# Performance work log

Measured on AMD Instinct MI355X. Metric: run time of the kernel, lower is better.

The kernel has to match this reference:

```python
import jax, jax.numpy as jnp
import numpy as np

B = 524288  # number of mel frames
MEL = 128   # mel bins (hard-coded in module)
D = 64      # code dim
K = 128     # codebook size


def setup_inputs() -> dict:
    key = jax.random.key(0)
    ks = jax.random.split(key, 7)
    return {
        "mel_frame": jax.random.normal(ks[0], (B, MEL), dtype=jnp.float32),
        "W_in": jax.random.normal(ks[1], (D, MEL), dtype=jnp.float32) * 0.05,
        "b_in": jax.random.normal(ks[2], (D,), dtype=jnp.float32) * 0.05,
        "cb0": jax.random.normal(ks[3], (K, D), dtype=jnp.float32),
        "cb1": jax.random.normal(ks[4], (K, D), dtype=jnp.float32),
        "W_out": jax.random.normal(ks[5], (MEL, D), dtype=jnp.float32) * 0.05,
        "b_out": jax.random.normal(ks[6], (MEL,), dtype=jnp.float32) * 0.05,
    }


def reference(mel_frame, W_in, b_in, cb0, cb1, W_out, b_out):
    # encode: project mel -> d, then greedy residual VQ over 2 codebooks
    z = mel_frame @ W_in.T + b_in                      # (B, D)
    residual = z
    z_q = jnp.zeros_like(z)
    idxs = []
    for cb in (cb0, cb1):
        # squared L2 distance without materializing (B, K, D):
        # ||r - c||^2 = ||r||^2 - 2 r.c + ||c||^2  -> (B, K)
        dist = (
            jnp.sum(residual * residual, axis=-1, keepdims=True)
            - 2.0 * (residual @ cb.T)
            + jnp.sum(cb * cb, axis=-1)
        )
        ind = jnp.argmin(dist, axis=-1)                # (B,)
        code = cb[ind]                                 # gather chosen codes (B, D)
        residual = residual - code
        z_q = z_q + code
        idxs.append(ind)
    # decode: sum of selected codes -> project back to mel
    mel = z_q @ W_out.T + b_out                        # (B, MEL)
    return mel, jnp.stack(idxs, axis=-1)
```

## Files before the change

### kernel.cpp

```cpp
#include <hip/hip_runtime.h>
#include <hip/hip_bf16.h>

#define B_ROWS   524288
#define MEL_BINS 128
#define DIM      64
#define KCODES   128

#define WS_WT 0
#define WS_P0 (WS_WT + MEL_BINS*DIM)
#define WS_P1 (WS_P0 + DIM*KCODES)
#define WS_N0 (WS_P1 + DIM*KCODES)
#define WS_N1 (WS_N0 + KCODES)
#define WS_T0 (WS_N1 + KCODES)
#define WS_T1 (WS_T0 + KCODES*MEL_BINS)
#define WS_TOT (WS_T1 + KCODES*MEL_BINS)

__device__ __forceinline__ float np_pairwise64_sq(const float* v) {
#pragma clang fp contract(off)
    float r0 = v[0]*v[0], r1 = v[1]*v[1], r2 = v[2]*v[2], r3 = v[3]*v[3];
    float r4 = v[4]*v[4], r5 = v[5]*v[5], r6 = v[6]*v[6], r7 = v[7]*v[7];
#pragma unroll
    for (int i = 8; i < 64; i += 8) {
        r0 += v[i+0]*v[i+0]; r1 += v[i+1]*v[i+1];
        r2 += v[i+2]*v[i+2]; r3 += v[i+3]*v[i+3];
        r4 += v[i+4]*v[i+4]; r5 += v[i+5]*v[i+5];
        r6 += v[i+6]*v[i+6]; r7 += v[i+7]*v[i+7];
    }
    return ((r0 + r1) + (r2 + r3)) + ((r4 + r5) + (r6 + r7));
}

__global__ __launch_bounds__(256) void rvq_precomp(
    const float* __restrict__ W_in, const float* __restrict__ cb0,
    const float* __restrict__ cb1, const float* __restrict__ W_out,
    float* __restrict__ ws)
{
#pragma clang fp contract(off)
    float* WT = ws + WS_WT;
    float* P0 = ws + WS_P0;
    float* P1 = ws + WS_P1;
    float* n0 = ws + WS_N0;
    float* n1 = ws + WS_N1;
    float* T0 = ws + WS_T0;
    float* T1 = ws + WS_T1;

    int tid = blockIdx.x * 256 + threadIdx.x;
    if (tid < 16384) {
        int i = tid >> 7, m = tid & 127;
        double a = 0.0;
        for (int d = 0; d < DIM; ++d)
            a = fma((double)cb0[i*DIM + d], (double)W_out[m*DIM + d], a);
        T0[tid] = (float)a;
    } else if (tid < 32768) {
        int t = tid - 16384;
        int i = t >> 7, m = t & 127;
        double a = 0.0;
        for (int d = 0; d < DIM; ++d)
            a = fma((double)cb1[i*DIM + d], (double)W_out[m*DIM + d], a);
        T1[t] = (float)a;
    } else if (tid < 40960) {
        int t = tid - 32768;
        int j = t >> 6, d = t & 63;
        WT[t] = W_in[d*MEL_BINS + j];
    } else if (tid < 41216) {
        int t = tid - 40960;
        const float* cb = (t & 128) ? cb1 : cb0;
        float*       nn = (t & 128) ? n1  : n0;
        int k = t & 127;
        nn[k] = np_pairwise64_sq(cb + k*DIM);
    } else if (tid < 49408) {
        int e = tid - 41216;
        int c = e >> 10, rem = e & 1023;
        int d = rem >> 4, t = rem & 15;
        P0[e] = cb0[(c*16 + t)*DIM + d];
    } else if (tid < 57600) {
        int e = tid - 49408;
        int c = e >> 10, rem = e & 1023;
        int d = rem >> 4, t = rem & 15;
        P1[e] = cb1[(c*16 + t)*DIM + d];
    }
}

__global__ __launch_bounds__(256) void rvq_main(
    const float* __restrict__ mel,
    const float* __restrict__ b_in,
    const float* __restrict__ cb0,
    const float* __restrict__ cb1,
    const float* __restrict__ b_out,
    const float* __restrict__ ws,
    float* __restrict__ out_mel,
    float* __restrict__ out_idx)
{
#pragma clang fp contract(off)
    const float* __restrict__ n0g = ws + WS_N0;
    const float* __restrict__ n1g = ws + WS_N1;
    const float* __restrict__ T0  = ws + WS_T0;
    const float* __restrict__ T1  = ws + WS_T1;

    __shared__ float slds[4096];
    float4* sw4 = reinterpret_cast<float4*>(slds);
    const float4* sl4 = reinterpret_cast<const float4*>(slds);

    const int tid = threadIdx.x;
    const int b = blockIdx.x * 256 + tid;
    const float4* melr = reinterpret_cast<const float4*>(mel + (size_t)b * MEL_BINS);

    float z[DIM];
#pragma unroll
    for (int d = 0; d < DIM; ++d) z[d] = 0.f;

    const float4* wt4 = reinterpret_cast<const float4*>(ws + WS_WT);
    for (int h = 0; h < 2; ++h) {
        __syncthreads();
#pragma unroll
        for (int i = 0; i < 4; ++i) sw4[i*256 + tid] = wt4[h*1024 + i*256 + tid];
        __syncthreads();

        for (int jc = 0; jc < 16; ++jc) {
            float4 m4 = melr[h*16 + jc];
#pragma unroll
            for (int seg = 0; seg < 4; ++seg) {
                float mj = (seg == 0) ? m4.x : (seg == 1) ? m4.y : (seg == 2) ? m4.z : m4.w;
                const float4* w4 = sl4 + (jc*4 + seg)*16;
#pragma unroll
                for (int q = 0; q < 16; ++q) {
                    float4 wv = w4[q];
                    z[4*q + 0] = fmaf(wv.x, mj, z[4*q + 0]);
                    z[4*q + 1] = fmaf(wv.y, mj, z[4*q + 1]);
                    z[4*q + 2] = fmaf(wv.z, mj, z[4*q + 2]);
                    z[4*q + 3] = fmaf(wv.w, mj, z[4*q + 3]);
                }
            }
        }
    }
#pragma unroll
    for (int d = 0; d < DIM; ++d) z[d] = z[d] + b_in[d];

    float s0 = z[0]*z[0], s1 = z[1]*z[1], s2 = z[2]*z[2], s3 = z[3]*z[3];
    float s4 = z[4]*z[4], s5 = z[5]*z[5], s6 = z[6]*z[6], s7 = z[7]*z[7];
#pragma unroll
    for (int i = 8; i < 64; i += 8) {
        s0 += z[i+0]*z[i+0]; s1 += z[i+1]*z[i+1];
        s2 += z[i+2]*z[i+2]; s3 += z[i+3]*z[i+3];
        s4 += z[i+4]*z[i+4]; s5 += z[i+5]*z[i+5];
        s6 += z[i+6]*z[i+6]; s7 += z[i+7]*z[i+7];
    }
    float sum_rr = ((s0 + s1) + (s2 + s3)) + ((s4 + s5) + (s6 + s7));

    const float4* p04 = reinterpret_cast<const float4*>(ws + WS_P0);
    float best0 = 3.4e38f; int i0 = 0;
    for (int h = 0; h < 2; ++h) {
        __syncthreads();
#pragma unroll
        for (int i = 0; i < 4; ++i) sw4[i*256 + tid] = p04[h*1024 + i*256 + tid];
        __syncthreads();

        for (int q = 0; q < 4; ++q) {
            const float4* pan = sl4 + q*256;
            float acc[16];
#pragma unroll
            for (int t = 0; t < 16; ++t) acc[t] = 0.f;
#pragma unroll
            for (int d = 0; d < DIM; ++d) {
                float4 p0 = pan[d*4 + 0];
                float4 p1 = pan[d*4 + 1];
                float4 p2 = pan[d*4 + 2];
                float4 p3 = pan[d*4 + 3];
                float zd = z[d];
                acc[ 0] = fmaf(p0.x, zd, acc[ 0]);
                acc[ 1] = fmaf(p0.y, zd, acc[ 1]);
                acc[ 2] = fmaf(p0.z, zd, acc[ 2]);
                acc[ 3] = fmaf(p0.w, zd, acc[ 3]);
                acc[ 4] = fmaf(p1.x, zd, acc[ 4]);
                acc[ 5] = fmaf(p1.y, zd, acc[ 5]);
                acc[ 6] = fmaf(p1.z, zd, acc[ 6]);
                acc[ 7] = fmaf(p1.w, zd, acc[ 7]);
                acc[ 8] = fmaf(p2.x, zd, acc[ 8]);
                acc[ 9] = fmaf(p2.y, zd, acc[ 9]);
                acc[10] = fmaf(p2.z, zd, acc[10]);
                acc[11] = fmaf(p2.w, zd, acc[11]);
                acc[12] = fmaf(p3.x, zd, acc[12]);
                acc[13] = fmaf(p3.y, zd, acc[13]);
                acc[14] = fmaf(p3.z, zd, acc[14]);
                acc[15] = fmaf(p3.w, zd, acc[15]);
            }
            const int kb = h*64 + q*16;
            const float* nk = n0g + kb;
#pragma unroll
            for (int t = 0; t < 16; ++t) {
                float dist = (sum_rr - 2.0f*acc[t]) + nk[t];
                if (dist < best0) { best0 = dist; i0 = kb + t; }
            }
        }
    }

    {
        const float* cc = cb0 + (size_t)i0 * DIM;
#pragma unroll
        for (int d = 0; d < DIM; ++d) z[d] = z[d] - cc[d];
    }

    s0 = z[0]*z[0]; s1 = z[1]*z[1]; s2 = z[2]*z[2]; s3 = z[3]*z[3];
    s4 = z[4]*z[4]; s5 = z[5]*z[5]; s6 = z[6]*z[6]; s7 = z[7]*z[7];
#pragma unroll
    for (int i = 8; i < 64; i += 8) {
        s0 += z[i+0]*z[i+0]; s1 += z[i+1]*z[i+1];
        s2 += z[i+2]*z[i+2]; s3 += z[i+3]*z[i+3];
        s4 += z[i+4]*z[i+4]; s5 += z[i+5]*z[i+5];
        s6 += z[i+6]*z[i+6]; s7 += z[i+7]*z[i+7];
    }
    sum_rr = ((s0 + s1) + (s2 + s3)) + ((s4 + s5) + (s6 + s7));

    const float4* p14 = reinterpret_cast<const float4*>(ws + WS_P1);
    float best1 = 3.4e38f; int i1 = 0;
    for (int h = 0; h < 2; ++h) {
        __syncthreads();
#pragma unroll
        for (int i = 0; i < 4; ++i) sw4[i*256 + tid] = p14[h*1024 + i*256 + tid];
        __syncthreads();

        for (int q = 0; q < 4; ++q) {
            const float4* pan = sl4 + q*256;
            float acc[16];
#pragma unroll
            for (int t = 0; t < 16; ++t) acc[t] = 0.f;
#pragma unroll
            for (int d = 0; d < DIM; ++d) {
                float4 p0 = pan[d*4 + 0];
                float4 p1 = pan[d*4 + 1];
                float4 p2 = pan[d*4 + 2];
                float4 p3 = pan[d*4 + 3];
                float zd = z[d];
                acc[ 0] = fmaf(p0.x, zd, acc[ 0]);
                acc[ 1] = fmaf(p0.y, zd, acc[ 1]);
                acc[ 2] = fmaf(p0.z, zd, acc[ 2]);
                acc[ 3] = fmaf(p0.w, zd, acc[ 3]);
                acc[ 4] = fmaf(p1.x, zd, acc[ 4]);
                acc[ 5] = fmaf(p1.y, zd, acc[ 5]);
                acc[ 6] = fmaf(p1.z, zd, acc[ 6]);
                acc[ 7] = fmaf(p1.w, zd, acc[ 7]);
                acc[ 8] = fmaf(p2.x, zd, acc[ 8]);
                acc[ 9] = fmaf(p2.y, zd, acc[ 9]);
                acc[10] = fmaf(p2.z, zd, acc[10]);
                acc[11] = fmaf(p2.w, zd, acc[11]);
                acc[12] = fmaf(p3.x, zd, acc[12]);
                acc[13] = fmaf(p3.y, zd, acc[13]);
                acc[14] = fmaf(p3.z, zd, acc[14]);
                acc[15] = fmaf(p3.w, zd, acc[15]);
            }
            const int kb = h*64 + q*16;
            const float* nk = n1g + kb;
#pragma unroll
            for (int t = 0; t < 16; ++t) {
                float dist = (sum_rr - 2.0f*acc[t]) + nk[t];
                if (dist < best1) { best1 = dist; i1 = kb + t; }
            }
        }
    }

    const float4* t0r = reinterpret_cast<const float4*>(T0 + (size_t)i0 * MEL_BINS);
    const float4* t1r = reinterpret_cast<const float4*>(T1 + (size_t)i1 * MEL_BINS);
    float4* outr = reinterpret_cast<float4*>(out_mel + (size_t)b * MEL_BINS);
#pragma unroll 4
    for (int q = 0; q < MEL_BINS / 4; ++q) {
        float4 a = t0r[q], cc = t1r[q];
        float4 o;
        o.x = a.x + cc.x + b_out[4*q + 0];
        o.y = a.y + cc.y + b_out[4*q + 1];
        o.z = a.z + cc.z + b_out[4*q + 2];
        o.w = a.w + cc.w + b_out[4*q + 3];
        outr[q] = o;
    }

    out_idx[2*(size_t)b + 0] = (float)i0;
    out_idx[2*(size_t)b + 1] = (float)i1;
}

extern "C" void kernel_launch(void* const* d_in, const int* in_sizes, int n_in,
                              void* d_out, int out_size, void* d_ws, size_t ws_size,
                              hipStream_t stream)
{
    const float* mel   = (const float*)d_in[0];
    const float* W_in  = (const float*)d_in[1];
    const float* b_in  = (const float*)d_in[2];
    const float* cb0   = (const float*)d_in[3];
    const float* cb1   = (const float*)d_in[4];
    const float* W_out = (const float*)d_in[5];
    const float* b_out = (const float*)d_in[6];

    float* ws      = (float*)d_ws;
    float* out_mel = (float*)d_out;
    float* out_idx = (float*)d_out + (size_t)B_ROWS * MEL_BINS;

    rvq_precomp<<<(WS_TOT + 255) / 256, 256, 0, stream>>>(W_in, cb0, cb1, W_out, ws);
    rvq_main<<<B_ROWS / 256, 256, 0, stream>>>(mel, b_in, cb0, cb1, b_out, ws,
                                               out_mel, out_idx);
}
```

Baseline: 516.5 us.

## Compute encoder projection in 16-dim chunks reading weights directly from global memory

The input projection no longer stages W_in^T through shared memory with block barriers. It loops over four 16-wide output-dim chunks, and each chunk re-reads the thread's mel row and takes uniform weight loads straight from the global workspace. This is meant to cut the live accumulator registers and remove the LDS staging and syncs, at the cost of reading the mel row four times, which relies on cache hits. The squared-norm reduction is folded into each chunk and rewritten with an 8-way accumulator array.

```diff
diff --git a/kernel.cpp b/kernel.cpp
--- a/kernel.cpp
+++ b/kernel.cpp
@@ -91,6 +91,7 @@
     float* __restrict__ out_idx)
 {
 #pragma clang fp contract(off)
+    const float* __restrict__ WTg = ws + WS_WT;
     const float* __restrict__ n0g = ws + WS_N0;
     const float* __restrict__ n1g = ws + WS_N1;
     const float* __restrict__ T0  = ws + WS_T0;
@@ -105,46 +106,37 @@
     const float4* melr = reinterpret_cast<const float4*>(mel + (size_t)b * MEL_BINS);
 
     float z[DIM];
-#pragma unroll
-    for (int d = 0; d < DIM; ++d) z[d] = 0.f;
-
-    const float4* wt4 = reinterpret_cast<const float4*>(ws + WS_WT);
-    for (int h = 0; h < 2; ++h) {
-        __syncthreads();
-#pragma unroll
-        for (int i = 0; i < 4; ++i) sw4[i*256 + tid] = wt4[h*1024 + i*256 + tid];
-        __syncthreads();
-
-        for (int jc = 0; jc < 16; ++jc) {
-            float4 m4 = melr[h*16 + jc];
-#pragma unroll
-            for (int seg = 0; seg < 4; ++seg) {
-                float mj = (seg == 0) ? m4.x : (seg == 1) ? m4.y : (seg == 2) ? m4.z : m4.w;
-                const float4* w4 = sl4 + (jc*4 + seg)*16;
-#pragma unroll
-                for (int q = 0; q < 16; ++q) {
-                    float4 wv = w4[q];
-                    z[4*q + 0] = fmaf(wv.x, mj, z[4*q + 0]);
-                    z[4*q + 1] = fmaf(wv.y, mj, z[4*q + 1]);
-                    z[4*q + 2] = fmaf(wv.z, mj, z[4*q + 2]);
-                    z[4*q + 3] = fmaf(wv.w, mj, z[4*q + 3]);
-                }
-            }
-        }
-    }
-#pragma unroll
-    for (int d = 0; d < DIM; ++d) z[d] = z[d] + b_in[d];
-
-    float s0 = z[0]*z[0], s1 = z[1]*z[1], s2 = z[2]*z[2], s3 = z[3]*z[3];
-    float s4 = z[4]*z[4], s5 = z[5]*z[5], s6 = z[6]*z[6], s7 = z[7]*z[7];
-#pragma unroll
-    for (int i = 8; i < 64; i += 8) {
-        s0 += z[i+0]*z[i+0]; s1 += z[i+1]*z[i+1];
-        s2 += z[i+2]*z[i+2]; s3 += z[i+3]*z[i+3];
-        s4 += z[i+4]*z[i+4]; s5 += z[i+5]*z[i+5];
-        s6 += z[i+6]*z[i+6]; s7 += z[i+7]*z[i+7];
-    }
-    float sum_rr = ((s0 + s1) + (s2 + s3)) + ((s4 + s5) + (s6 + s7));
+    float r8[8];
+#pragma unroll
+    for (int t = 0; t < 8; ++t) r8[t] = 0.f;
+
+#pragma unroll
+    for (int db = 0; db < 4; ++db) {
+        float zz[16];
+#pragma unroll
+        for (int t = 0; t < 16; ++t) zz[t] = 0.f;
+
+        for (int jc = 0; jc < 32; ++jc) {
+            float4 m4 = melr[jc];
+            const float* w = WTg + jc * 4 * DIM + db * 16;
+#pragma unroll
+            for (int t = 0; t < 16; ++t) zz[t] = fmaf(w[t],         m4.x, zz[t]);
+#pragma unroll
+            for (int t = 0; t < 16; ++t) zz[t] = fmaf(w[DIM + t],   m4.y, zz[t]);
+#pragma unroll
+            for (int t = 0; t < 16; ++t) zz[t] = fmaf(w[2*DIM + t], m4.z, zz[t]);
+#pragma unroll
+            for (int t = 0; t < 16; ++t) zz[t] = fmaf(w[3*DIM + t], m4.w, zz[t]);
+        }
+#pragma unroll
+        for (int t = 0; t < 16; ++t) {
+            float v = zz[t] + b_in[db*16 + t];
+            z[db*16 + t] = v;
+            r8[t & 7] += v * v;
+        }
+        asm volatile("" ::: "memory");
+    }
+    float sum_rr = ((r8[0] + r8[1]) + (r8[2] + r8[3])) + ((r8[4] + r8[5]) + (r8[6] + r8[7]));
 
     const float4* p04 = reinterpret_cast<const float4*>(ws + WS_P0);
     float best0 = 3.4e38f; int i0 = 0;
@@ -199,16 +191,14 @@
         for (int d = 0; d < DIM; ++d) z[d] = z[d] - cc[d];
     }
 
-    s0 = z[0]*z[0]; s1 = z[1]*z[1]; s2 = z[2]*z[2]; s3 = z[3]*z[3];
-    s4 = z[4]*z[4]; s5 = z[5]*z[5]; s6 = z[6]*z[6]; s7 = z[7]*z[7];
-#pragma unroll
-    for (int i = 8; i < 64; i += 8) {
-        s0 += z[i+0]*z[i+0]; s1 += z[i+1]*z[i+1];
-        s2 += z[i+2]*z[i+2]; s3 += z[i+3]*z[i+3];
-        s4 += z[i+4]*z[i+4]; s5 += z[i+5]*z[i+5];
-        s6 += z[i+6]*z[i+6]; s7 += z[i+7]*z[i+7];
-    }
-    sum_rr = ((s0 + s1) + (s2 + s3)) + ((s4 + s5) + (s6 + s7));
+#pragma unroll
+    for (int t = 0; t < 8; ++t) r8[t] = 0.f;
+#pragma unroll
+    for (int i = 0; i < 64; i += 8) {
+#pragma unroll
+        for (int t = 0; t < 8; ++t) r8[t] += z[i + t] * z[i + t];
+    }
+    sum_rr = ((r8[0] + r8[1]) + (r8[2] + r8[3])) + ((r8[4] + r8[5]) + (r8[6] + r8[7]));
 
     const float4* p14 = reinterpret_cast<const float4*>(ws + WS_P1);
     float best1 = 3.4e38f; int i1 = 0;
```

After: 865.8 us. 67.6% more time.

## Split codebook operands between LDS and scalar global loads

Applied to the files above, without the earlier changes.

Each codebook is now split into two halves. Half the codes per 16-code chunk are staged in LDS, and the other half are read through uniform (scalar) global loads from the workspace. This removes the second LDS staging pass and its barriers, and halves LDS read traffic in the distance loops, moving that bandwidth onto the scalar memory path instead. The risk is added latency from scalar loads inside the hot FMA loop, plus higher SGPR pressure.

```diff
diff --git a/kernel.cpp b/kernel.cpp
--- a/kernel.cpp
+++ b/kernel.cpp
@@ -6,13 +6,15 @@
 #define DIM      64
 #define KCODES   128
 
-#define WS_WT 0
-#define WS_P0 (WS_WT + MEL_BINS*DIM)
-#define WS_P1 (WS_P0 + DIM*KCODES)
-#define WS_N0 (WS_P1 + DIM*KCODES)
-#define WS_N1 (WS_N0 + KCODES)
-#define WS_T0 (WS_N1 + KCODES)
-#define WS_T1 (WS_T0 + KCODES*MEL_BINS)
+#define WS_WT  0
+#define WS_PL0 (WS_WT + 8192)
+#define WS_PS0 (WS_PL0 + 4096)
+#define WS_PL1 (WS_PS0 + 4096)
+#define WS_PS1 (WS_PL1 + 4096)
+#define WS_N0  (WS_PS1 + 4096)
+#define WS_N1  (WS_N0 + KCODES)
+#define WS_T0  (WS_N1 + KCODES)
+#define WS_T1  (WS_T0 + KCODES*MEL_BINS)
 #define WS_TOT (WS_T1 + KCODES*MEL_BINS)
 
 __device__ __forceinline__ float np_pairwise64_sq(const float* v) {
@@ -35,13 +37,15 @@
     float* __restrict__ ws)
 {
 #pragma clang fp contract(off)
-    float* WT = ws + WS_WT;
-    float* P0 = ws + WS_P0;
-    float* P1 = ws + WS_P1;
-    float* n0 = ws + WS_N0;
-    float* n1 = ws + WS_N1;
-    float* T0 = ws + WS_T0;
-    float* T1 = ws + WS_T1;
+    float* WT  = ws + WS_WT;
+    float* PL0 = ws + WS_PL0;
+    float* PS0 = ws + WS_PS0;
+    float* PL1 = ws + WS_PL1;
+    float* PS1 = ws + WS_PS1;
+    float* n0  = ws + WS_N0;
+    float* n1  = ws + WS_N1;
+    float* T0  = ws + WS_T0;
+    float* T1  = ws + WS_T1;
 
     int tid = blockIdx.x * 256 + threadIdx.x;
     if (tid < 16384) {
@@ -69,14 +73,20 @@
         nn[k] = np_pairwise64_sq(cb + k*DIM);
     } else if (tid < 49408) {
         int e = tid - 41216;
-        int c = e >> 10, rem = e & 1023;
-        int d = rem >> 4, t = rem & 15;
-        P0[e] = cb0[(c*16 + t)*DIM + d];
+        int half = e >> 12;
+        int x = e & 4095;
+        int c = x >> 9, rem = x & 511;
+        int d = rem >> 3, t = rem & 7;
+        if (half == 0) PL0[x] = cb0[(16*c + t)*DIM + d];
+        else           PS0[x] = cb0[(16*c + 8 + t)*DIM + d];
     } else if (tid < 57600) {
         int e = tid - 49408;
-        int c = e >> 10, rem = e & 1023;
-        int d = rem >> 4, t = rem & 15;
-        P1[e] = cb1[(c*16 + t)*DIM + d];
+        int half = e >> 12;
+        int x = e & 4095;
+        int c = x >> 9, rem = x & 511;
+        int d = rem >> 3, t = rem & 7;
+        if (half == 0) PL1[x] = cb1[(16*c + t)*DIM + d];
+        else           PS1[x] = cb1[(16*c + 8 + t)*DIM + d];
     }
 }
 
@@ -91,10 +101,12 @@
     float* __restrict__ out_idx)
 {
 #pragma clang fp contract(off)
-    const float* __restrict__ n0g = ws + WS_N0;
-    const float* __restrict__ n1g = ws + WS_N1;
-    const float* __restrict__ T0  = ws + WS_T0;
-    const float* __restrict__ T1  = ws + WS_T1;
+    const float* __restrict__ ps0g = ws + WS_PS0;
+    const float* __restrict__ ps1g = ws + WS_PS1;
+    const float* __restrict__ n0g  = ws + WS_N0;
+    const float* __restrict__ n1g  = ws + WS_N1;
+    const float* __restrict__ T0   = ws + WS_T0;
+    const float* __restrict__ T1   = ws + WS_T1;
 
     __shared__ float slds[4096];
     float4* sw4 = reinterpret_cast<float4*>(slds);
@@ -146,50 +158,48 @@
     }
     float sum_rr = ((s0 + s1) + (s2 + s3)) + ((s4 + s5) + (s6 + s7));
 
-    const float4* p04 = reinterpret_cast<const float4*>(ws + WS_P0);
+    const float4* pl04 = reinterpret_cast<const float4*>(ws + WS_PL0);
     float best0 = 3.4e38f; int i0 = 0;
-    for (int h = 0; h < 2; ++h) {
-        __syncthreads();
-#pragma unroll
-        for (int i = 0; i < 4; ++i) sw4[i*256 + tid] = p04[h*1024 + i*256 + tid];
-        __syncthreads();
-
-        for (int q = 0; q < 4; ++q) {
-            const float4* pan = sl4 + q*256;
-            float acc[16];
-#pragma unroll
-            for (int t = 0; t < 16; ++t) acc[t] = 0.f;
-#pragma unroll
-            for (int d = 0; d < DIM; ++d) {
-                float4 p0 = pan[d*4 + 0];
-                float4 p1 = pan[d*4 + 1];
-                float4 p2 = pan[d*4 + 2];
-                float4 p3 = pan[d*4 + 3];
-                float zd = z[d];
-                acc[ 0] = fmaf(p0.x, zd, acc[ 0]);
-                acc[ 1] = fmaf(p0.y, zd, acc[ 1]);
-                acc[ 2] = fmaf(p0.z, zd, acc[ 2]);
-                acc[ 3] = fmaf(p0.w, zd, acc[ 3]);
-                acc[ 4] = fmaf(p1.x, zd, acc[ 4]);
-                acc[ 5] = fmaf(p1.y, zd, acc[ 5]);
-                acc[ 6] = fmaf(p1.z, zd, acc[ 6]);
-                acc[ 7] = fmaf(p1.w, zd, acc[ 7]);
-                acc[ 8] = fmaf(p2.x, zd, acc[ 8]);
-                acc[ 9] = fmaf(p2.y, zd, acc[ 9]);
-                acc[10] = fmaf(p2.z, zd, acc[10]);
-                acc[11] = fmaf(p2.w, zd, acc[11]);
-                acc[12] = fmaf(p3.x, zd, acc[12]);
-                acc[13] = fmaf(p3.y, zd, acc[13]);
-                acc[14] = fmaf(p3.z, zd, acc[14]);
-                acc[15] = fmaf(p3.w, zd, acc[15]);
-            }
-            const int kb = h*64 + q*16;
-            const float* nk = n0g + kb;
-#pragma unroll
-            for (int t = 0; t < 16; ++t) {
-                float dist = (sum_rr - 2.0f*acc[t]) + nk[t];
-                if (dist < best0) { best0 = dist; i0 = kb + t; }
-            }
+    __syncthreads();
+#pragma unroll
+    for (int i = 0; i < 4; ++i) sw4[i*256 + tid] = pl04[i*256 + tid];
+    __syncthreads();
+
+    for (int c = 0; c < 8; ++c) {
+        const float4* pan  = sl4 + c*128;
+        const float* srow  = ps0g + c*512;
+        float acc[16];
+#pragma unroll
+        for (int t = 0; t < 16; ++t) acc[t] = 0.f;
+#pragma unroll
+        for (int d = 0; d < DIM; ++d) {
+            float4 p0 = pan[d*2 + 0];
+            float4 p1 = pan[d*2 + 1];
+            const float* sr = srow + d*8;
+            float zd = z[d];
+            acc[ 0] = fmaf(p0.x, zd, acc[ 0]);
+            acc[ 1] = fmaf(p0.y, zd, acc[ 1]);
+            acc[ 2] = fmaf(p0.z, zd, acc[ 2]);
+            acc[ 3] = fmaf(p0.w, zd, acc[ 3]);
+            acc[ 4] = fmaf(p1.x, zd, acc[ 4]);
+            acc[ 5] = fmaf(p1.y, zd, acc[ 5]);
+            acc[ 6] = fmaf(p1.z, zd, acc[ 6]);
+            acc[ 7] = fmaf(p1.w, zd, acc[ 7]);
+            acc[ 8] = fmaf(sr[0], zd, acc[ 8]);
+            acc[ 9] = fmaf(sr[1], zd, acc[ 9]);
+            acc[10] = fmaf(sr[2], zd, acc[10]);
+            acc[11] = fmaf(sr[3], zd, acc[11]);
+            acc[12] = fmaf(sr[4], zd, acc[12]);
+            acc[13] = fmaf(sr[5], zd, acc[13]);
+            acc[14] = fmaf(sr[6], zd, acc[14]);
+            acc[15] = fmaf(sr[7], zd, acc[15]);
+        }
+        const int kb = c*16;
+        const float* nk = n0g + kb;
+#pragma unroll
+        for (int t = 0; t < 16; ++t) {
+            float dist = (sum_rr - 2.0f*acc[t]) + nk[t];
+            if (dist < best0) { best0 = dist; i0 = kb + t; }
         }
     }
 
@@ -210,50 +220,48 @@
     }
     sum_rr = ((s0 + s1) + (s2 + s3)) + ((s4 + s5) + (s6 + s7));
 
-    const float4* p14 = reinterpret_cast<const float4*>(ws + WS_P1);
+    const float4* pl14 = reinterpret_cast<const float4*>(ws + WS_PL1);
     float best1 = 3.4e38f; int i1 = 0;
-    for (int h = 0; h < 2; ++h) {
-        __syncthreads();
-#pragma unroll
-        for (int i = 0; i < 4; ++i) sw4[i*256 + tid] = p14[h*1024 + i*256 + tid];
-        __syncthreads();
-
-        for (int q = 0; q < 4; ++q) {
-            const float4* pan = sl4 + q*256;
-            float acc[16];
-#pragma unroll
-            for (int t = 0; t < 16; ++t) acc[t] = 0.f;
-#pragma unroll
-            for (int d = 0; d < DIM; ++d) {
-                float4 p0 = pan[d*4 + 0];
-                float4 p1 = pan[d*4 + 1];
-                float4 p2 = pan[d*4 + 2];
-                float4 p3 = pan[d*4 + 3];
-                float zd = z[d];
-                acc[ 0] = fmaf(p0.x, zd, acc[ 0]);
-                acc[ 1] = fmaf(p0.y, zd, acc[ 1]);
-                acc[ 2] = fmaf(p0.z, zd, acc[ 2]);
-                acc[ 3] = fmaf(p0.w, zd, acc[ 3]);
-                acc[ 4] = fmaf(p1.x, zd, acc[ 4]);
-                acc[ 5] = fmaf(p1.y, zd, acc[ 5]);
-                acc[ 6] = fmaf(p1.z, zd, acc[ 6]);
-                acc[ 7] = fmaf(p1.w, zd, acc[ 7]);
-                acc[ 8] = fmaf(p2.x, zd, acc[ 8]);
-                acc[ 9] = fmaf(p2.y, zd, acc[ 9]);
-                acc[10] = fmaf(p2.z, zd, acc[10]);
-                acc[11] = fmaf(p2.w, zd, acc[11]);
-                acc[12] = fmaf(p3.x, zd, acc[12]);
-                acc[13] = fmaf(p3.y, zd, acc[13]);
-                acc[14] = fmaf(p3.z, zd, acc[14]);
-                acc[15] = fmaf(p3.w, zd, acc[15]);
-            }
-            const int kb = h*64 + q*16;
-            const float* nk = n1g + kb;
-#pragma unroll
-            for (int t = 0; t < 16; ++t) {
-                float dist = (sum_rr - 2.0f*acc[t]) + nk[t];
-                if (dist < best1) { best1 = dist; i1 = kb + t; }
-            }
+    __syncthreads();
+#pragma unroll
+    for (int i = 0; i < 4; ++i) sw4[i*256 + tid] = pl14[i*256 + tid];
+    __syncthreads();
+
+    for (int c = 0; c < 8; ++c) {
+        const float4* pan  = sl4 + c*128;
+        const float* srow  = ps1g + c*512;
+        float acc[16];
+#pragma unroll
+        for (int t = 0; t < 16; ++t) acc[t] = 0.f;
+#pragma unroll
+        for (int d = 0; d < DIM; ++d) {
+            float4 p0 = pan[d*2 + 0];
+            float4 p1 = pan[d*2 + 1];
+            const float* sr = srow + d*8;
+            float zd = z[d];
+            acc[ 0] = fmaf(p0.x, zd, acc[ 0]);
+            acc[ 1] = fmaf(p0.y, zd, acc[ 1]);
+            acc[ 2] = fmaf(p0.z, zd, acc[ 2]);
+            acc[ 3] = fmaf(p0.w, zd, acc[ 3]);
+            acc[ 4] = fmaf(p1.x, zd, acc[ 4]);
+            acc[ 5] = fmaf(p1.y, zd, acc[ 5]);
+            acc[ 6] = fmaf(p1.z, zd, acc[ 6]);
+            acc[ 7] = fmaf(p1.w, zd, acc[ 7]);
+            acc[ 8] = fmaf(sr[0], zd, acc[ 8]);
+            acc[ 9] = fmaf(sr[1], zd, acc[ 9]);
+            acc[10] = fmaf(sr[2], zd, acc[10]);
+            acc[11] = fmaf(sr[3], zd, acc[11]);
+            acc[12] = fmaf(sr[4], zd, acc[12]);
+            acc[13] = fmaf(sr[5], zd, acc[13]);
+            acc[14] = fmaf(sr[6], zd, acc[14]);
+            acc[15] = fmaf(sr[7], zd, acc[15]);
+        }
+        const int kb = c*16;
+        const float* nk = n1g + kb;
+#pragma unroll
+        for (int t = 0; t < 16; ++t) {
+            float dist = (sum_rr - 2.0f*acc[t]) + nk[t];
+            if (dist < best1) { best1 = dist; i1 = kb + t; }
         }
     }
 
```

After: 485.0 us. -6.1%, faster.
